# Kernel optimization log

Hardware: AMD Instinct MI355X
Metric: run time of the kernel (lower is better)

## Reference

```python
import jax, jax.numpy as jnp
import numpy as np


def setup_inputs() -> dict:
    key = jax.random.key(0)
    feature = jax.random.normal(key, (32, 64, 128, 128), dtype=jnp.float32)
    return {"feature": feature}


def reference(feature):
    # feature: [B, C, H, W]
    B, C, H, W = feature.shape
    mgr = feature.mean()  # global mean over all elements

    # Per-(sample, channel) argmax location; row-major first-occurrence matches
    # the original strict '>' scan.
    flat_idx = jnp.argmax(feature.reshape(B, C, H * W), axis=-1)  # [B, C]
    max_x = flat_idx // W  # row index
    max_y = flat_idx % W   # col index

    i = jnp.arange(H)
    j = jnp.arange(W)
    # squared distance from each pixel to its channel's argmax: [B, C, H, W]
    dist2 = ((max_x[:, :, None, None] - i[None, None, :, None]) ** 2
             + (max_y[:, :, None, None] - j[None, None, None, :]) ** 2)
    dist2 = dist2.astype(feature.dtype)

    f2 = feature * feature
    dis_loss = jnp.sum(f2 * dist2)

    # max over OTHER channels at each pixel: top-2 over channel axis,
    # use 2nd max only for the channel that is the (first) argmax.
    t = jnp.moveaxis(feature, 1, -1)  # [B, H, W, C]
    top2, _ = jax.lax.top_k(t, 2)    # [B, H, W, 2]
    m1 = top2[..., 0][:, None, :, :]  # [B, 1, H, W]
    m2 = top2[..., 1][:, None, :, :]
    amax_c = jnp.argmax(t, axis=-1)[:, None, :, :]  # [B, 1, H, W]
    c_ids = jnp.arange(C)[None, :, None, None]      # [1, C, 1, 1]
    max_others = jnp.where(c_ids == amax_c, m2, m1)  # [B, C, H, W]

    div_loss = jnp.sum(f2 * (max_others - mgr) ** 2)

    n = B * C * H * W
    return dis_loss / n, div_loss / n
```

## Files before the change

### kernel.cpp

```cpp
#include <hip/hip_runtime.h>

#define HW     16384
#define WDIM   128
#define HDIM   128
#define CDIM   64
#define BDIM   32
#define CHUNKS 128
#define NBF    (BDIM * CHUNKS)
#define NBC    (BDIM * CDIM)


#define OFF_WMAX  0
#define OFF_WIDX  (1u << 20)
#define OFF_WSF   (2u << 20)
#define OFF_WS0   (3u << 20)
#define OFF_WSJ   (4u << 20)
#define OFF_WSQJ  (5u << 20)
#define OFF_WA1   (6u << 20)
#define OFF_WA2   ((6u << 20) + 32768u)
#define OFF_K3    ((6u << 20) + 65536u)

__global__ __launch_bounds__(256) void f_fused(const float* __restrict__ feat,
                                               float* __restrict__ wmax, int* __restrict__ widx,
                                               float* __restrict__ wsf,  float* __restrict__ ws0,
                                               float* __restrict__ wsj,  float* __restrict__ wsqj,
                                               double* __restrict__ wa1, double* __restrict__ wa2) {
    __shared__ float tile[CDIM * 129];
    __shared__ float sc2[128 * 3];
    __shared__ float ared[128 * 2];
    __shared__ float scb[4 * 64 * 7];

    const int t  = threadIdx.x;
    const int bf = blockIdx.x;
    const int b  = bf >> 7, row = bf & 127;
    const float* src = feat + (size_t)b * CDIM * HW + (size_t)row * WDIM;

    float4 buf[8];
    #pragma unroll
    for (int k = 0; k < 8; ++k) {
        int idx = k * 256 + t;
        int c = idx >> 5, g = idx & 31;
        buf[k] = *(const float4*)(src + (size_t)c * HW + g * 4);
    }
    #pragma unroll
    for (int k = 0; k < 8; ++k) {
        int idx = k * 256 + t;
        int c = idx >> 5, g = idx & 31;
        float* dst = &tile[c * 129 + g * 4];
        dst[0] = buf[k].x; dst[1] = buf[k].y; dst[2] = buf[k].z; dst[3] = buf[k].w;
    }
    __syncthreads();

    {
        const int px = t & 127, half = t >> 7;
        float m1 = -INFINITY, m2 = -INFINITY, s2 = 0.f;
        #pragma unroll
        for (int cc = 0; cc < 32; ++cc) {
            float x = tile[(half * 32 + cc) * 129 + px];
            if (x > m1) { m2 = m1; m1 = x; } else { m2 = fmaxf(m2, x); }
            s2 = fmaf(x, x, s2);
        }
        if (half) { sc2[px * 3] = m1; sc2[px * 3 + 1] = m2; sc2[px * 3 + 2] = s2; }
        __syncthreads();
        if (!half) {
            float n1 = sc2[px * 3], n2 = sc2[px * 3 + 1], s2b = sc2[px * 3 + 2];
            float mm1 = fmaxf(m1, n1);
            float mm2 = fmaxf(fminf(m1, n1), fmaxf(m2, n2));
            float S2 = s2 + s2b;
            float q = mm1 * mm1, r = S2 - q;
            ared[px * 2]     = q * r + mm2 * mm2 * q;
            ared[px * 2 + 1] = mm1 * r + mm2 * q;
        }
        __syncthreads();
        for (int off = 64; off > 0; off >>= 1) {
            if (t < off) {
                ared[t * 2]     += ared[(t + off) * 2];
                ared[t * 2 + 1] += ared[(t + off) * 2 + 1];
            }
            __syncthreads();
        }
        if (t == 0) { wa1[bf] = (double)ared[0]; wa2[bf] = (double)ared[1]; }
    }

    {
        const int ch = t & 63, sub = t >> 6;
        const int p0 = sub * 32;
        float bm = -INFINITY; int bpx = 0;
        float sf = 0.f, s0 = 0.f, sj = 0.f, sqj = 0.f;
        #pragma unroll
        for (int i = 0; i < 32; ++i) {
            int p = p0 + i;
            float x = tile[ch * 129 + p];
            if (x > bm) { bm = x; bpx = p; }
            sf += x;
            float q = x * x;
            s0 += q;
            sj  = fmaf(q, (float)p, sj);
            sqj = fmaf(q, (float)(p * p), sqj);
        }
        int o = (sub * 64 + ch) * 7;
        scb[o] = bm; scb[o + 1] = __int_as_float(bpx);
        scb[o + 2] = sf; scb[o + 3] = s0; scb[o + 4] = sj; scb[o + 5] = sqj;
        __syncthreads();
        if (t < 64) {
            float M = -INFINITY; int P = 0;
            float SF = 0.f, S0 = 0.f, SJ = 0.f, SQ = 0.f;
            #pragma unroll
            for (int s = 0; s < 4; ++s) {
                int oo = (s * 64 + t) * 7;
                float m = scb[oo];
                if (m > M) { M = m; P = __float_as_int(scb[oo + 1]); }
                SF += scb[oo + 2]; S0 += scb[oo + 3];
                SJ += scb[oo + 4]; SQ += scb[oo + 5];
            }
            int out = bf * 64 + t;
            wmax[out] = M; widx[out] = P;
            wsf[out] = SF; ws0[out] = S0; wsj[out] = SJ; wsqj[out] = SQ;
        }
    }
}

__global__ __launch_bounds__(128) void k3_channel(const float* __restrict__ wmax, const int* __restrict__ widx,
                                                  const float* __restrict__ wsf,  const float* __restrict__ ws0,
                                                  const float* __restrict__ wsj,  const float* __restrict__ wsqj,
                                                  double* __restrict__ k3out) {
    const int bc = blockIdx.x;
    const int b = bc >> 6, c = bc & 63;
    const int t = threadIdx.x;
    const int idx = (b * 128 + t) * 64 + c;

    float m = wmax[idx]; int px = widx[idx];
    float sf = wsf[idx], s0 = ws0[idx], sj = wsj[idx], sqj = wsqj[idx];

    __shared__ float rm[128]; __shared__ int rr[128]; __shared__ int rp[128];
    rm[t] = m; rr[t] = t; rp[t] = px;
    __syncthreads();
    for (int off = 64; off > 0; off >>= 1) {
        if (t < off) {
            float mo = rm[t + off];
            if (mo > rm[t] || (mo == rm[t] && rr[t + off] < rr[t])) {
                rm[t] = mo; rr[t] = rr[t + off]; rp[t] = rp[t + off];
            }
        }
        __syncthreads();
    }
    const int mi = rr[0], mj = rp[0];

    double di = (double)(mi - t);
    double disc = (di * di + (double)mj * (double)mj) * (double)s0
                - 2.0 * (double)mj * (double)sj + (double)sqj;

    __shared__ double rd[128], rsf[128], rs0[128];
    rd[t] = disc; rsf[t] = (double)sf; rs0[t] = (double)s0;
    __syncthreads();
    for (int off = 64; off > 0; off >>= 1) {
        if (t < off) { rd[t] += rd[t + off]; rsf[t] += rsf[t + off]; rs0[t] += rs0[t + off]; }
        __syncthreads();
    }
    if (t == 0) {
        k3out[bc * 3]     = rsf[0];
        k3out[bc * 3 + 1] = rs0[0];
        k3out[bc * 3 + 2] = rd[0];
    }
}

__global__ __launch_bounds__(256) void k4_final(const double* __restrict__ k3out,
                                                const double* __restrict__ wa1,
                                                const double* __restrict__ wa2,
                                                float* __restrict__ out) {
    const int t = threadIdx.x;
    double sf = 0, s0 = 0, dis = 0, a1 = 0, a2 = 0;
    for (int i = t; i < NBC; i += 256) {
        sf += k3out[i * 3]; s0 += k3out[i * 3 + 1]; dis += k3out[i * 3 + 2];
    }
    for (int i = t; i < NBF; i += 256) { a1 += wa1[i]; a2 += wa2[i]; }

    __shared__ double r[5][256];
    r[0][t] = sf; r[1][t] = s0; r[2][t] = dis; r[3][t] = a1; r[4][t] = a2;
    __syncthreads();
    for (int off = 128; off > 0; off >>= 1) {
        if (t < off) {
            #pragma unroll
            for (int q = 0; q < 5; ++q) r[q][t] += r[q][t + off];
        }
        __syncthreads();
    }
    if (t == 0) {
        const double n = 33554432.0;
        double mgr = r[0][0] / n;
        out[0] = (float)(r[2][0] / n);
        out[1] = (float)((r[3][0] - 2.0 * mgr * r[4][0] + mgr * mgr * r[1][0]) / n);
    }
}

extern "C" void kernel_launch(void* const* d_in, const int* in_sizes, int n_in,
                              void* d_out, int out_size, void* d_ws, size_t ws_size,
                              hipStream_t stream) {
    const float* feat = (const float*)d_in[0];
    float* out = (float*)d_out;
    char* ws = (char*)d_ws;

    float*  wmax = (float*)(ws + OFF_WMAX);
    int*    widx = (int*)  (ws + OFF_WIDX);
    float*  wsf  = (float*)(ws + OFF_WSF);
    float*  ws0  = (float*)(ws + OFF_WS0);
    float*  wsj  = (float*)(ws + OFF_WSJ);
    float*  wsqj = (float*)(ws + OFF_WSQJ);
    double* wa1  = (double*)(ws + OFF_WA1);
    double* wa2  = (double*)(ws + OFF_WA2);
    double* k3o  = (double*)(ws + OFF_K3);

    f_fused<<<NBF, 256, 0, stream>>>(feat, wmax, widx, wsf, ws0, wsj, wsqj, wa1, wa2);
    k3_channel<<<NBC, 128, 0, stream>>>(wmax, widx, wsf, ws0, wsj, wsqj, k3o);
    k4_final<<<1, 256, 0, stream>>>(k3o, wa1, wa2, out);
}
```

Measured before the change: 54.97 us.

## Cut barriers with wave-shuffle reduction, merge shared scratch, transpose partial layout

```diff
diff --git a/kernel.cpp b/kernel.cpp
--- a/kernel.cpp
+++ b/kernel.cpp
@@ -2,13 +2,10 @@
 
 #define HW     16384
 #define WDIM   128
-#define HDIM   128
 #define CDIM   64
 #define BDIM   32
-#define CHUNKS 128
-#define NBF    (BDIM * CHUNKS)
-#define NBC    (BDIM * CDIM)
-
+#define NBF    4096
+#define NBC    2048
 
 #define OFF_WMAX  0
 #define OFF_WIDX  (1u << 20)
@@ -20,15 +17,14 @@
 #define OFF_WA2   ((6u << 20) + 32768u)
 #define OFF_K3    ((6u << 20) + 65536u)
 
-__global__ __launch_bounds__(256) void f_fused(const float* __restrict__ feat,
-                                               float* __restrict__ wmax, int* __restrict__ widx,
-                                               float* __restrict__ wsf,  float* __restrict__ ws0,
-                                               float* __restrict__ wsj,  float* __restrict__ wsqj,
-                                               double* __restrict__ wa1, double* __restrict__ wa2) {
+__global__ __launch_bounds__(256, 4) void f_fused(const float* __restrict__ feat,
+                                                  float* __restrict__ wmax, int* __restrict__ widx,
+                                                  float* __restrict__ wsf,  float* __restrict__ ws0,
+                                                  float* __restrict__ wsj,  float* __restrict__ wsqj,
+                                                  double* __restrict__ wa1, double* __restrict__ wa2) {
     __shared__ float tile[CDIM * 129];
-    __shared__ float sc2[128 * 3];
-    __shared__ float ared[128 * 2];
-    __shared__ float scb[4 * 64 * 7];
+    __shared__ float scratch[1792];
+    __shared__ float sred[4];
 
     const int t  = threadIdx.x;
     const int bf = blockIdx.x;
@@ -51,72 +47,78 @@
     }
     __syncthreads();
 
+    const int px = t & 127, half = t >> 7;
+    float m1 = -INFINITY, m2 = -INFINITY, s2 = 0.f;
+    #pragma unroll
+    for (int cc = 0; cc < 32; ++cc) {
+        float x = tile[(half * 32 + cc) * 129 + px];
+        if (x > m1) { m2 = m1; m1 = x; } else { m2 = fmaxf(m2, x); }
+        s2 = fmaf(x, x, s2);
+    }
+    if (half) { scratch[px * 3] = m1; scratch[px * 3 + 1] = m2; scratch[px * 3 + 2] = s2; }
+    __syncthreads();
+
+    const int ch = t & 63, sub = t >> 6, p0 = sub * 32;
+    float bm = -INFINITY; int bi = 0;
+    float sf = 0.f, s0 = 0.f, sjl = 0.f, sql = 0.f;
+    #pragma unroll
+    for (int i = 0; i < 32; ++i) {
+        float x = tile[ch * 129 + p0 + i];
+        if (x > bm) { bm = x; bi = i; }
+        sf += x;
+        float q = x * x;
+        s0 += q;
+        sjl = fmaf(q, (float)i, sjl);
+        sql = fmaf(q, (float)(i * i), sql);
+    }
+
+    if (!half) {
+        float n1 = scratch[px * 3], n2 = scratch[px * 3 + 1], s2b = scratch[px * 3 + 2];
+        float mm1 = fmaxf(m1, n1);
+        float mm2 = fmaxf(fminf(m1, n1), fmaxf(m2, n2));
+        float S2 = s2 + s2b;
+        float qq = mm1 * mm1, rr = S2 - qq;
+        float a1 = qq * rr + mm2 * mm2 * qq;
+        float a2 = mm1 * rr + mm2 * qq;
+        #pragma unroll
+        for (int off = 32; off > 0; off >>= 1) {
+            a1 += __shfl_down(a1, off);
+            a2 += __shfl_down(a2, off);
+        }
+        if (t == 0)  { sred[0] = a1; sred[1] = a2; }
+        if (t == 64) { sred[2] = a1; sred[3] = a2; }
+    }
+    __syncthreads();
+
     {
-        const int px = t & 127, half = t >> 7;
-        float m1 = -INFINITY, m2 = -INFINITY, s2 = 0.f;
+        float sj  = fmaf((float)p0, s0, sjl);
+        float sqj = fmaf((float)(p0 * p0), s0, fmaf(2.f * (float)p0, sjl, sql));
+        int o = (sub * 64 + ch) * 7;
+        scratch[o]     = bm;
+        scratch[o + 1] = __int_as_float(p0 + bi);
+        scratch[o + 2] = sf; scratch[o + 3] = s0;
+        scratch[o + 4] = sj; scratch[o + 5] = sqj;
+    }
+    if (t == 255) {
+        wa1[bf] = (double)(sred[0] + sred[2]);
+        wa2[bf] = (double)(sred[1] + sred[3]);
+    }
+    __syncthreads();
+
+    if (t < 64) {
+        float M = -INFINITY; int P = 0;
+        float SF = 0.f, S0 = 0.f, SJ = 0.f, SQ = 0.f;
         #pragma unroll
-        for (int cc = 0; cc < 32; ++cc) {
-            float x = tile[(half * 32 + cc) * 129 + px];
-            if (x > m1) { m2 = m1; m1 = x; } else { m2 = fmaxf(m2, x); }
-            s2 = fmaf(x, x, s2);
-        }
-        if (half) { sc2[px * 3] = m1; sc2[px * 3 + 1] = m2; sc2[px * 3 + 2] = s2; }
-        __syncthreads();
-        if (!half) {
-            float n1 = sc2[px * 3], n2 = sc2[px * 3 + 1], s2b = sc2[px * 3 + 2];
-            float mm1 = fmaxf(m1, n1);
-            float mm2 = fmaxf(fminf(m1, n1), fmaxf(m2, n2));
-            float S2 = s2 + s2b;
-            float q = mm1 * mm1, r = S2 - q;
-            ared[px * 2]     = q * r + mm2 * mm2 * q;
-            ared[px * 2 + 1] = mm1 * r + mm2 * q;
-        }
-        __syncthreads();
-        for (int off = 64; off > 0; off >>= 1) {
-            if (t < off) {
-                ared[t * 2]     += ared[(t + off) * 2];
-                ared[t * 2 + 1] += ared[(t + off) * 2 + 1];
-            }
-            __syncthreads();
-        }
-        if (t == 0) { wa1[bf] = (double)ared[0]; wa2[bf] = (double)ared[1]; }
-    }
-
-    {
-        const int ch = t & 63, sub = t >> 6;
-        const int p0 = sub * 32;
-        float bm = -INFINITY; int bpx = 0;
-        float sf = 0.f, s0 = 0.f, sj = 0.f, sqj = 0.f;
-        #pragma unroll
-        for (int i = 0; i < 32; ++i) {
-            int p = p0 + i;
-            float x = tile[ch * 129 + p];
-            if (x > bm) { bm = x; bpx = p; }
-            sf += x;
-            float q = x * x;
-            s0 += q;
-            sj  = fmaf(q, (float)p, sj);
-            sqj = fmaf(q, (float)(p * p), sqj);
-        }
-        int o = (sub * 64 + ch) * 7;
-        scb[o] = bm; scb[o + 1] = __int_as_float(bpx);
-        scb[o + 2] = sf; scb[o + 3] = s0; scb[o + 4] = sj; scb[o + 5] = sqj;
-        __syncthreads();
-        if (t < 64) {
-            float M = -INFINITY; int P = 0;
-            float SF = 0.f, S0 = 0.f, SJ = 0.f, SQ = 0.f;
-            #pragma unroll
-            for (int s = 0; s < 4; ++s) {
-                int oo = (s * 64 + t) * 7;
-                float m = scb[oo];
-                if (m > M) { M = m; P = __float_as_int(scb[oo + 1]); }
-                SF += scb[oo + 2]; S0 += scb[oo + 3];
-                SJ += scb[oo + 4]; SQ += scb[oo + 5];
-            }
-            int out = bf * 64 + t;
-            wmax[out] = M; widx[out] = P;
-            wsf[out] = SF; ws0[out] = S0; wsj[out] = SJ; wsqj[out] = SQ;
-        }
+        for (int s = 0; s < 4; ++s) {
+            int oo = (s * 64 + t) * 7;
+            float m = scratch[oo];
+            if (m > M) { M = m; P = __float_as_int(scratch[oo + 1]); }
+            SF += scratch[oo + 2]; S0 += scratch[oo + 3];
+            SJ += scratch[oo + 4]; SQ += scratch[oo + 5];
+        }
+        int out = t * 4096 + bf;
+        wmax[out] = M; widx[out] = P;
+        wsf[out] = SF; ws0[out] = S0; wsj[out] = SJ; wsqj[out] = SQ;
     }
 }
 
@@ -127,7 +129,7 @@
     const int bc = blockIdx.x;
     const int b = bc >> 6, c = bc & 63;
     const int t = threadIdx.x;
-    const int idx = (b * 128 + t) * 64 + c;
+    const int idx = c * 4096 + b * 128 + t;
 
     float m = wmax[idx]; int px = widx[idx];
     float sf = wsf[idx], s0 = ws0[idx], sj = wsj[idx], sqj = wsqj[idx];
```

Measured after the change: 53.69 us. 2.3% less time.
